# Performance work log

Measured on AMD Instinct MI355X. Metric: run time of the kernel, lower is better.

## Reference

```python
import jax, jax.numpy as jnp
import numpy as np

N_NODES = 50000
N_EDGES = 800000
D_IN = 128
D_HID = 128
D_OUT = 1
N_LAYERS = 3


def _sage_conv(x, src, dst, Wl, bl, Wr):
    # PyG SAGEConv (mean aggr): out = lin_l(mean_{j in N(i)} x_j) + lin_r(x_i)
    n = x.shape[0]
    msg = x[src]                                              # [E, F] gather
    s = jax.ops.segment_sum(msg, dst, num_segments=n)         # [N, F]
    cnt = jax.ops.segment_sum(jnp.ones((src.shape[0],), x.dtype), dst, num_segments=n)
    mean = s / jnp.maximum(cnt, 1.0)[:, None]
    return mean @ Wl.T + bl + x @ Wr.T


def setup_inputs() -> dict:
    key = jax.random.key(0)
    ks = jax.random.split(key, 2 + 3 * N_LAYERS + 2)
    x = jax.random.normal(ks[0], (N_NODES, D_IN), dtype=jnp.float32)
    edge_index = jax.random.randint(ks[1], (2, N_EDGES), 0, N_NODES, dtype=jnp.int64)
    inp = {"x": x, "edge_index": edge_index}
    dims_in = [D_IN] + [D_HID] * (N_LAYERS - 1)
    for i in range(N_LAYERS):
        fi = dims_in[i]
        sc = 1.0 / np.sqrt(fi)
        inp[f"Wl{i}"] = jax.random.uniform(ks[2 + 3 * i], (D_HID, fi), jnp.float32, -sc, sc)
        inp[f"bl{i}"] = jax.random.uniform(ks[3 + 3 * i], (D_HID,), jnp.float32, -sc, sc)
        inp[f"Wr{i}"] = jax.random.uniform(ks[4 + 3 * i], (D_HID, fi), jnp.float32, -sc, sc)
    sc = 1.0 / np.sqrt(D_HID)
    inp["Wf"] = jax.random.uniform(ks[-2], (D_OUT, D_HID), jnp.float32, -sc, sc)
    inp["bf"] = jax.random.uniform(ks[-1], (D_OUT,), jnp.float32, -sc, sc)
    return inp


def reference(x, edge_index, Wl0, bl0, Wr0, Wl1, bl1, Wr1, Wl2, bl2, Wr2, Wf, bf):
    src, dst = edge_index[0], edge_index[1]
    h = x
    # dropout is identity in eval mode (F.dropout with training=False)
    for Wl, bl, Wr in ((Wl0, bl0, Wr0), (Wl1, bl1, Wr1), (Wl2, bl2, Wr2)):
        h = jax.nn.relu(_sage_conv(h, src, dst, Wl, bl, Wr))
    return h @ Wf.T + bf
```

## Files before the change

### kernel.cpp

```cpp
#include <hip/hip_runtime.h>
#include <hip/hip_bf16.h>


constexpr int NN = 50000;
constexpr int NE = 800000;
constexpr int NTILE = NN / 16;
constexpr int EPB = 4096;
constexpr int NBLK = (NE + EPB - 1) / EPB;
constexpr int NBUCK = 196;
constexpr int BCAP = 6144;

using bf16x8 = __attribute__((ext_vector_type(8))) short;
using f32x4  = __attribute__((ext_vector_type(4))) float;

__device__ __forceinline__ unsigned short bf16_rne(float f) {
    unsigned u = __float_as_uint(f);
    unsigned r = (u + 0x7FFFu + ((u >> 16) & 1u)) >> 16;
    return (unsigned short)r;
}
__device__ __forceinline__ float bf16_f(unsigned short h) {
    return __uint_as_float(((unsigned)h) << 16);
}
__device__ __forceinline__ unsigned pack_split(float v) {
    unsigned short hi = bf16_rne(v);
    float r = v - bf16_f(hi);
    unsigned short lo = bf16_rne(r);
    return (((unsigned)hi) << 16) | (unsigned)lo;
}


__global__ __launch_bounds__(256) void k_hist(const int* __restrict__ ei,
                                              int* __restrict__ hist) {
    __shared__ int h[256];
    h[threadIdx.x] = 0;
    __syncthreads();
    int e0 = blockIdx.x * EPB;
    int e1 = e0 + EPB; if (e1 > NE) e1 = NE;
    for (int e = e0 + threadIdx.x; e < e1; e += 256)
        atomicAdd(&h[ei[NE + e] >> 8], 1);
    __syncthreads();
    hist[blockIdx.x * 256 + threadIdx.x] = h[threadIdx.x];
}

__global__ __launch_bounds__(256) void k_colscan(int* __restrict__ hist,
                                                 int* __restrict__ tot) {
    __shared__ int ws[4];
    int b = blockIdx.x;
    int t = threadIdx.x;
    int orig = (t < NBLK) ? hist[t * 256 + b] : 0;
    int v = orig;
    int lane = t & 63, wave = t >> 6;
    for (int o = 1; o < 64; o <<= 1) { int u = __shfl_up(v, o); if (lane >= o) v += u; }
    if (lane == 63) ws[wave] = v;
    __syncthreads();
    int off = 0;
    for (int w = 0; w < wave; ++w) off += ws[w];
    int st = v + off - orig;
    if (t < NBLK) hist[t * 256 + b] = st;
    if (t == 255) tot[b] = st + orig;
}

__global__ __launch_bounds__(256) void k_total(const int* __restrict__ tot,
                                               int* __restrict__ dbase) {
    __shared__ int ws[4];
    int t = threadIdx.x;
    int orig = tot[t];
    int v = orig;
    int lane = t & 63, wave = t >> 6;
    for (int o = 1; o < 64; o <<= 1) { int u = __shfl_up(v, o); if (lane >= o) v += u; }
    if (lane == 63) ws[wave] = v;
    __syncthreads();
    int off = 0;
    for (int w = 0; w < wave; ++w) off += ws[w];
    dbase[t] = v + off - orig;
    if (t == 255) dbase[256] = v + off;
}

__global__ __launch_bounds__(256) void k_addbase(int* __restrict__ hist,
                                                 const int* __restrict__ dbase) {
    hist[blockIdx.x * 256 + threadIdx.x] += dbase[threadIdx.x];
}

__global__ __launch_bounds__(256) void k_scatter1(const int* __restrict__ ei,
                                                  const int* __restrict__ hist,
                                                  unsigned* __restrict__ packed) {
    __shared__ int cur[256];
    cur[threadIdx.x] = hist[blockIdx.x * 256 + threadIdx.x];
    __syncthreads();
    int e0 = blockIdx.x * EPB;
    int e1 = e0 + EPB; if (e1 > NE) e1 = NE;
    for (int e = e0 + threadIdx.x; e < e1; e += 256) {
        int s = ei[e];
        int d = ei[NE + e];
        int pos = atomicAdd(&cur[d >> 8], 1);
        packed[pos] = ((unsigned)d << 16) | (unsigned)s;
    }
}

__global__ __launch_bounds__(256) void k_bucket_csr(const unsigned* __restrict__ packed,
        const int* __restrict__ dbase, unsigned short* __restrict__ perm,
        int* __restrict__ cnt, int* __restrict__ row_start) {
    __shared__ unsigned recs[BCAP];
    __shared__ unsigned short outs[BCAP];
    __shared__ int cntL[256];
    __shared__ int ws[4];
    int b = blockIdx.x;
    int lo = dbase[b];
    int m = dbase[b + 1] - lo;
    if (m > BCAP) m = BCAP;
    int t = threadIdx.x;
    cntL[t] = 0;
    __syncthreads();
    for (int i = t; i < m; i += 256) {
        unsigned r = packed[lo + i];
        recs[i] = r;
        atomicAdd(&cntL[(r >> 16) & 255], 1);
    }
    __syncthreads();
    int lane = t & 63, wave = t >> 6;
    int orig = cntL[t], v = orig;
    for (int o = 1; o < 64; o <<= 1) { int u = __shfl_up(v, o); if (lane >= o) v += u; }
    if (lane == 63) ws[wave] = v;
    __syncthreads();
    int off = 0;
    for (int w = 0; w < wave; ++w) off += ws[w];
    int st = v + off - orig;
    int node = b * 256 + t;
    if (node < NN) { cnt[node] = orig; row_start[node] = lo + st; }
    __syncthreads();
    cntL[t] = st;
    __syncthreads();
    for (int i = t; i < m; i += 256) {
        unsigned r = recs[i];
        int pos = atomicAdd(&cntL[(r >> 16) & 255], 1);
        outs[pos] = (unsigned short)(r & 0xFFFFu);
    }
    __syncthreads();
    for (int i = t; i < m; i += 256)
        perm[lo + i] = outs[i];
}


__global__ void k_pack_x(const float* __restrict__ x,
                         unsigned short* __restrict__ hhi,
                         unsigned short* __restrict__ hlo) {
    int i = blockIdx.x * blockDim.x + threadIdx.x;
    constexpr int TOT = NN * 128 / 4;
    if (i < TOT) {
        float4 v = ((const float4*)x)[i];
        unsigned p0 = pack_split(v.x), p1 = pack_split(v.y);
        unsigned p2 = pack_split(v.z), p3 = pack_split(v.w);
        uint2 hi, lo;
        hi.x = (p0 >> 16) | (p1 & 0xFFFF0000u);
        hi.y = (p2 >> 16) | (p3 & 0xFFFF0000u);
        lo.x = (p0 & 0xFFFFu) | (p1 << 16);
        lo.y = (p2 & 0xFFFFu) | (p3 << 16);
        ((uint2*)hhi)[i] = hi;
        ((uint2*)hlo)[i] = lo;
    }
}

__global__ void k_pack_w(const float* __restrict__ Wl, const float* __restrict__ Wr,
                         unsigned short* __restrict__ whi, unsigned short* __restrict__ wlo) {
    int i = blockIdx.x * blockDim.x + threadIdx.x;
    if (i < 128 * 256) {
        int c = i >> 8;
        int k = i & 255;
        float v = (k < 128) ? Wl[c * 128 + k] : Wr[c * 128 + (k - 128)];
        unsigned short hi = bf16_rne(v);
        whi[i] = hi;
        wlo[i] = bf16_rne(v - bf16_f(hi));
    }
}

__global__ void k_init_out(float* __restrict__ out, const float* __restrict__ bf) {
    int i = blockIdx.x * blockDim.x + threadIdx.x;
    if (i < NN) out[i] = bf[0];
}

__global__ __launch_bounds__(256) void k_aggregate(const unsigned short* __restrict__ hhi,
        const int* __restrict__ row_start, const int* __restrict__ cnt,
        const unsigned short* __restrict__ perm,
        unsigned short* __restrict__ shi, unsigned short* __restrict__ slo) {
    int wave = __builtin_amdgcn_readfirstlane(threadIdx.x >> 6);
    int lane = threadIdx.x & 63;
    int node = blockIdx.x * 4 + wave;
    if (node >= NN) return;
    int deg = cnt[node];
    int start = row_start[node];
    const unsigned* base = (const unsigned*)hhi;
    float ax = 0.f, ay = 0.f;
    int j = 0;
    for (; j + 16 <= deg; j += 16) {
        int s[16];
#pragma unroll
        for (int u = 0; u < 16; ++u) s[u] = perm[start + j + u];
        unsigned q[16];
#pragma unroll
        for (int u = 0; u < 16; ++u) q[u] = base[(size_t)s[u] * 64 + lane];
#pragma unroll
        for (int u = 0; u < 16; ++u) {
            ax += __uint_as_float(q[u] << 16);
            ay += __uint_as_float(q[u] & 0xFFFF0000u);
        }
    }
    for (; j + 4 <= deg; j += 4) {
        int s[4];
#pragma unroll
        for (int u = 0; u < 4; ++u) s[u] = perm[start + j + u];
        unsigned q[4];
#pragma unroll
        for (int u = 0; u < 4; ++u) q[u] = base[(size_t)s[u] * 64 + lane];
#pragma unroll
        for (int u = 0; u < 4; ++u) {
            ax += __uint_as_float(q[u] << 16);
            ay += __uint_as_float(q[u] & 0xFFFF0000u);
        }
    }
    for (; j < deg; ++j) {
        int s = perm[start + j];
        unsigned q = base[(size_t)s * 64 + lane];
        ax += __uint_as_float(q << 16);
        ay += __uint_as_float(q & 0xFFFF0000u);
    }
    float inv = 1.0f / (float)(deg > 1 ? deg : 1);
    unsigned p0 = pack_split(ax * inv);
    unsigned p1 = pack_split(ay * inv);
    ((unsigned*)shi)[(size_t)node * 64 + lane] = (p0 >> 16) | (p1 & 0xFFFF0000u);
    ((unsigned*)slo)[(size_t)node * 64 + lane] = (p0 & 0xFFFFu) | (p1 << 16);
}

__global__ __launch_bounds__(256, 2) void k_gemm_ws(
        const unsigned short* __restrict__ Ahi0, const unsigned short* __restrict__ Alo0,
        const unsigned short* __restrict__ Ahi1, const unsigned short* __restrict__ Alo1,
        const unsigned short* __restrict__ Whi, const unsigned short* __restrict__ Wlo,
        const float* __restrict__ bias,
        unsigned short* __restrict__ Ohi, unsigned short* __restrict__ Olo) {
    int wave = __builtin_amdgcn_readfirstlane(threadIdx.x >> 6);
    int lane = threadIdx.x & 63;
    int row = lane & 15;
    int kb = lane >> 4;
    int ct0 = wave * 2;

    bf16x8 bh[2][8], bl[2][8];
#pragma unroll
    for (int c = 0; c < 2; ++c)
#pragma unroll
        for (int kc = 0; kc < 8; ++kc) {
            size_t widx = (size_t)((ct0 + c) * 16 + row) * 256 + kc * 32 + kb * 8;
            bh[c][kc] = *(const bf16x8*)(Whi + widx);
            bl[c][kc] = *(const bf16x8*)(Wlo + widx);
        }
    float b0 = bias[ct0 * 16 + row];
    float b1 = bias[ct0 * 16 + 16 + row];

    for (int t = blockIdx.x; t < NTILE; t += gridDim.x) {
        int n0 = t * 16;
        size_t rb = (size_t)(n0 + row) * 128 + kb * 8;
        bf16x8 ah[8], al[8];
#pragma unroll
        for (int kc = 0; kc < 4; ++kc) {
            ah[kc] = *(const bf16x8*)(Ahi0 + rb + kc * 32);
            al[kc] = *(const bf16x8*)(Alo0 + rb + kc * 32);
        }
#pragma unroll
        for (int kc = 0; kc < 4; ++kc) {
            ah[4 + kc] = *(const bf16x8*)(Ahi1 + rb + kc * 32);
            al[4 + kc] = *(const bf16x8*)(Alo1 + rb + kc * 32);
        }
        f32x4 acc0 = {0.f, 0.f, 0.f, 0.f};
        f32x4 acc1 = {0.f, 0.f, 0.f, 0.f};
#pragma unroll
        for (int kc = 0; kc < 8; ++kc) {
            acc0 = __builtin_amdgcn_mfma_f32_16x16x32_bf16(ah[kc], bh[0][kc], acc0, 0, 0, 0);
            acc0 = __builtin_amdgcn_mfma_f32_16x16x32_bf16(al[kc], bh[0][kc], acc0, 0, 0, 0);
            acc0 = __builtin_amdgcn_mfma_f32_16x16x32_bf16(ah[kc], bl[0][kc], acc0, 0, 0, 0);
            acc1 = __builtin_amdgcn_mfma_f32_16x16x32_bf16(ah[kc], bh[1][kc], acc1, 0, 0, 0);
            acc1 = __builtin_amdgcn_mfma_f32_16x16x32_bf16(al[kc], bh[1][kc], acc1, 0, 0, 0);
            acc1 = __builtin_amdgcn_mfma_f32_16x16x32_bf16(ah[kc], bl[1][kc], acc1, 0, 0, 0);
        }
        __syncthreads();
        int cb0 = ct0 * 16 + row;
#pragma unroll
        for (int r = 0; r < 4; ++r) {
            int n = n0 + kb * 4 + r;
            size_t ro = (size_t)n * 128;
            unsigned p0 = pack_split(fmaxf(acc0[r] + b0, 0.f));
            unsigned p1 = pack_split(fmaxf(acc1[r] + b1, 0.f));
            Ohi[ro + cb0]      = (unsigned short)(p0 >> 16);
            Olo[ro + cb0]      = (unsigned short)(p0 & 0xFFFFu);
            Ohi[ro + cb0 + 16] = (unsigned short)(p1 >> 16);
            Olo[ro + cb0 + 16] = (unsigned short)(p1 & 0xFFFFu);
        }
    }
}

__global__ __launch_bounds__(256, 2) void k_gemm_head(
        const unsigned short* __restrict__ Ahi0, const unsigned short* __restrict__ Alo0,
        const unsigned short* __restrict__ Ahi1, const unsigned short* __restrict__ Alo1,
        const unsigned short* __restrict__ Whi, const unsigned short* __restrict__ Wlo,
        const float* __restrict__ bias, const float* __restrict__ Wf,
        float* __restrict__ out) {
    int wave = __builtin_amdgcn_readfirstlane(threadIdx.x >> 6);
    int lane = threadIdx.x & 63;
    int row = lane & 15;
    int kb = lane >> 4;
    int ct0 = wave * 2;

    bf16x8 bh[2][8], bl[2][8];
#pragma unroll
    for (int c = 0; c < 2; ++c)
#pragma unroll
        for (int kc = 0; kc < 8; ++kc) {
            size_t widx = (size_t)((ct0 + c) * 16 + row) * 256 + kc * 32 + kb * 8;
            bh[c][kc] = *(const bf16x8*)(Whi + widx);
            bl[c][kc] = *(const bf16x8*)(Wlo + widx);
        }
    float b0 = bias[ct0 * 16 + row];
    float b1 = bias[ct0 * 16 + 16 + row];
    float w0 = Wf[ct0 * 16 + row];
    float w1 = Wf[ct0 * 16 + 16 + row];

    for (int t = blockIdx.x; t < NTILE; t += gridDim.x) {
        int n0 = t * 16;
        size_t rb = (size_t)(n0 + row) * 128 + kb * 8;
        bf16x8 ah[8], al[8];
#pragma unroll
        for (int kc = 0; kc < 4; ++kc) {
            ah[kc] = *(const bf16x8*)(Ahi0 + rb + kc * 32);
            al[kc] = *(const bf16x8*)(Alo0 + rb + kc * 32);
        }
#pragma unroll
        for (int kc = 0; kc < 4; ++kc) {
            ah[4 + kc] = *(const bf16x8*)(Ahi1 + rb + kc * 32);
            al[4 + kc] = *(const bf16x8*)(Alo1 + rb + kc * 32);
        }
        f32x4 acc0 = {0.f, 0.f, 0.f, 0.f};
        f32x4 acc1 = {0.f, 0.f, 0.f, 0.f};
#pragma unroll
        for (int kc = 0; kc < 8; ++kc) {
            acc0 = __builtin_amdgcn_mfma_f32_16x16x32_bf16(ah[kc], bh[0][kc], acc0, 0, 0, 0);
            acc0 = __builtin_amdgcn_mfma_f32_16x16x32_bf16(al[kc], bh[0][kc], acc0, 0, 0, 0);
            acc0 = __builtin_amdgcn_mfma_f32_16x16x32_bf16(ah[kc], bl[0][kc], acc0, 0, 0, 0);
            acc1 = __builtin_amdgcn_mfma_f32_16x16x32_bf16(ah[kc], bh[1][kc], acc1, 0, 0, 0);
            acc1 = __builtin_amdgcn_mfma_f32_16x16x32_bf16(al[kc], bh[1][kc], acc1, 0, 0, 0);
            acc1 = __builtin_amdgcn_mfma_f32_16x16x32_bf16(ah[kc], bl[1][kc], acc1, 0, 0, 0);
        }
        float part[4];
#pragma unroll
        for (int r = 0; r < 4; ++r)
            part[r] = fmaxf(acc0[r] + b0, 0.f) * w0 + fmaxf(acc1[r] + b1, 0.f) * w1;
#pragma unroll
        for (int o = 1; o < 16; o <<= 1) {
#pragma unroll
            for (int r = 0; r < 4; ++r) part[r] += __shfl_xor(part[r], o);
        }
        if (row == 0) {
#pragma unroll
            for (int r = 0; r < 4; ++r) atomicAdd(&out[n0 + kb * 4 + r], part[r]);
        }
    }
}

extern "C" void kernel_launch(void* const* d_in, const int* in_sizes, int n_in,
                              void* d_out, int out_size, void* d_ws, size_t ws_size,
                              hipStream_t stream) {
    const float* x   = (const float*)d_in[0];
    const int*   ei  = (const int*)d_in[1];
    const float* Wl0 = (const float*)d_in[2];
    const float* bl0 = (const float*)d_in[3];
    const float* Wr0 = (const float*)d_in[4];
    const float* Wl1 = (const float*)d_in[5];
    const float* bl1 = (const float*)d_in[6];
    const float* Wr1 = (const float*)d_in[7];
    const float* Wl2 = (const float*)d_in[8];
    const float* bl2 = (const float*)d_in[9];
    const float* Wr2 = (const float*)d_in[10];
    const float* Wf  = (const float*)d_in[11];
    const float* bf  = (const float*)d_in[12];
    float* out = (float*)d_out;

    char* p = (char*)d_ws;
    auto alloc = [&](size_t n) { void* r = (void*)p; p += (n + 255) & ~(size_t)255; return r; };
    int*            hist      = (int*)alloc((size_t)NBLK * 256 * 4);
    int*            tot       = (int*)alloc(256 * 4);
    int*            dbase     = (int*)alloc(257 * 4);
    int*            cnt       = (int*)alloc((size_t)NN * 4);
    int*            row_start = (int*)alloc((size_t)NN * 4);
    unsigned short* perm      = (unsigned short*)alloc((size_t)NE * 2);
    unsigned short* s_hi      = (unsigned short*)alloc((size_t)NN * 128 * 2);
    unsigned short* s_lo      = (unsigned short*)alloc((size_t)NN * 128 * 2);
    unsigned short* h_hi      = (unsigned short*)alloc((size_t)NN * 128 * 2);
    unsigned short* h_lo      = (unsigned short*)alloc((size_t)NN * 128 * 2);
    unsigned short* whi       = (unsigned short*)alloc((size_t)3 * 128 * 256 * 2);
    unsigned short* wlo       = (unsigned short*)alloc((size_t)3 * 128 * 256 * 2);
    unsigned*       packed    = (unsigned*)s_hi;

    dim3 b256(256);
    k_hist<<<dim3(NBLK), b256, 0, stream>>>(ei, hist);
    k_colscan<<<dim3(256), b256, 0, stream>>>(hist, tot);
    k_total<<<dim3(1), b256, 0, stream>>>(tot, dbase);
    k_addbase<<<dim3(NBLK), b256, 0, stream>>>(hist, dbase);
    k_scatter1<<<dim3(NBLK), b256, 0, stream>>>(ei, hist, packed);
    k_bucket_csr<<<dim3(NBUCK), b256, 0, stream>>>(packed, dbase, perm, cnt, row_start);

    k_pack_x<<<dim3((NN * 128 / 4 + 255) / 256), b256, 0, stream>>>(x, h_hi, h_lo);
    k_pack_w<<<dim3(128), b256, 0, stream>>>(Wl0, Wr0, whi + 0 * 32768, wlo + 0 * 32768);
    k_pack_w<<<dim3(128), b256, 0, stream>>>(Wl1, Wr1, whi + 1 * 32768, wlo + 1 * 32768);
    k_pack_w<<<dim3(128), b256, 0, stream>>>(Wl2, Wr2, whi + 2 * 32768, wlo + 2 * 32768);
    k_init_out<<<dim3((NN + 255) / 256), b256, 0, stream>>>(out, bf);

    dim3 gAgg((NN + 3) / 4);
    dim3 gGemm(512);

    k_aggregate<<<gAgg, b256, 0, stream>>>(h_hi, row_start, cnt, perm, s_hi, s_lo);
    k_gemm_ws<<<gGemm, b256, 0, stream>>>(s_hi, s_lo, h_hi, h_lo,
                                          whi + 0 * 32768, wlo + 0 * 32768, bl0, h_hi, h_lo);
    k_aggregate<<<gAgg, b256, 0, stream>>>(h_hi, row_start, cnt, perm, s_hi, s_lo);
    k_gemm_ws<<<gGemm, b256, 0, stream>>>(s_hi, s_lo, h_hi, h_lo,
                                          whi + 1 * 32768, wlo + 1 * 32768, bl1, h_hi, h_lo);
    k_aggregate<<<gAgg, b256, 0, stream>>>(h_hi, row_start, cnt, perm, s_hi, s_lo);
    k_gemm_head<<<gGemm, b256, 0, stream>>>(s_hi, s_lo, h_hi, h_lo,
                                            whi + 2 * 32768, wlo + 2 * 32768, bl2, Wf, out);
}
```

Baseline: 334.5 us.

## Use fixed-capacity atomic buckets and padded vectorized neighbor gather in aggregation

The CSR build drops the histogram, column-scan, total and add-base kernels. Each edge block now reserves space in fixed-capacity per-bucket regions through global atomics, staging records in shared memory, and the output init is folded into a new init kernel. Neighbor lists are padded to multiples of eight using a zeroed sentinel row at index NN. This lets the aggregate kernel read neighbor indices as 16-byte vectors and have each half-wave gather a different neighbor with 8-byte loads, combining the halves with a cross-lane shuffle. The aim is fewer launches and fewer, wider memory instructions in the gather, at the cost of redundant gathers of the padding row and a reliance on bucket sizes staying under the fixed capacity.

```diff
diff --git a/kernel.cpp b/kernel.cpp
--- a/kernel.cpp
+++ b/kernel.cpp
@@ -9,6 +9,7 @@
 constexpr int NBLK = (NE + EPB - 1) / EPB;
 constexpr int NBUCK = 196;
 constexpr int BCAP = 6144;
+constexpr int PCAP = 6144;
 
 using bf16x8 = __attribute__((ext_vector_type(8))) short;
 using f32x4  = __attribute__((ext_vector_type(4))) float;
@@ -29,88 +30,57 @@
 }
 
 
-__global__ __launch_bounds__(256) void k_hist(const int* __restrict__ ei,
-                                              int* __restrict__ hist) {
+__global__ __launch_bounds__(256) void k_init(float* __restrict__ out,
+        const float* __restrict__ bf, int* __restrict__ bcnt,
+        unsigned short* __restrict__ hhi) {
+    int i = blockIdx.x * blockDim.x + threadIdx.x;
+    if (i < NN) out[i] = bf[0];
+    if (i < 256) bcnt[i] = 0;
+    if (i < 128) hhi[(size_t)NN * 128 + i] = 0;
+}
+
+
+__global__ __launch_bounds__(256) void k_build_buckets(const int* __restrict__ ei,
+        int* __restrict__ bcnt, unsigned* __restrict__ packed) {
+    __shared__ unsigned stage[EPB];
     __shared__ int h[256];
-    h[threadIdx.x] = 0;
+    __shared__ int cur[256];
+    int t = threadIdx.x;
+    h[t] = 0;
     __syncthreads();
     int e0 = blockIdx.x * EPB;
     int e1 = e0 + EPB; if (e1 > NE) e1 = NE;
-    for (int e = e0 + threadIdx.x; e < e1; e += 256)
-        atomicAdd(&h[ei[NE + e] >> 8], 1);
-    __syncthreads();
-    hist[blockIdx.x * 256 + threadIdx.x] = h[threadIdx.x];
-}
-
-__global__ __launch_bounds__(256) void k_colscan(int* __restrict__ hist,
-                                                 int* __restrict__ tot) {
-    __shared__ int ws[4];
-    int b = blockIdx.x;
-    int t = threadIdx.x;
-    int orig = (t < NBLK) ? hist[t * 256 + b] : 0;
-    int v = orig;
-    int lane = t & 63, wave = t >> 6;
-    for (int o = 1; o < 64; o <<= 1) { int u = __shfl_up(v, o); if (lane >= o) v += u; }
-    if (lane == 63) ws[wave] = v;
-    __syncthreads();
-    int off = 0;
-    for (int w = 0; w < wave; ++w) off += ws[w];
-    int st = v + off - orig;
-    if (t < NBLK) hist[t * 256 + b] = st;
-    if (t == 255) tot[b] = st + orig;
-}
-
-__global__ __launch_bounds__(256) void k_total(const int* __restrict__ tot,
-                                               int* __restrict__ dbase) {
-    __shared__ int ws[4];
-    int t = threadIdx.x;
-    int orig = tot[t];
-    int v = orig;
-    int lane = t & 63, wave = t >> 6;
-    for (int o = 1; o < 64; o <<= 1) { int u = __shfl_up(v, o); if (lane >= o) v += u; }
-    if (lane == 63) ws[wave] = v;
-    __syncthreads();
-    int off = 0;
-    for (int w = 0; w < wave; ++w) off += ws[w];
-    dbase[t] = v + off - orig;
-    if (t == 255) dbase[256] = v + off;
-}
-
-__global__ __launch_bounds__(256) void k_addbase(int* __restrict__ hist,
-                                                 const int* __restrict__ dbase) {
-    hist[blockIdx.x * 256 + threadIdx.x] += dbase[threadIdx.x];
-}
-
-__global__ __launch_bounds__(256) void k_scatter1(const int* __restrict__ ei,
-                                                  const int* __restrict__ hist,
-                                                  unsigned* __restrict__ packed) {
-    __shared__ int cur[256];
-    cur[threadIdx.x] = hist[blockIdx.x * 256 + threadIdx.x];
-    __syncthreads();
-    int e0 = blockIdx.x * EPB;
-    int e1 = e0 + EPB; if (e1 > NE) e1 = NE;
-    for (int e = e0 + threadIdx.x; e < e1; e += 256) {
+    for (int e = e0 + t; e < e1; e += 256) {
         int s = ei[e];
         int d = ei[NE + e];
-        int pos = atomicAdd(&cur[d >> 8], 1);
-        packed[pos] = ((unsigned)d << 16) | (unsigned)s;
+        stage[e - e0] = ((unsigned)d << 16) | (unsigned)s;
+        atomicAdd(&h[d >> 8], 1);
+    }
+    __syncthreads();
+    if (t < NBUCK) cur[t] = t * BCAP + atomicAdd(&bcnt[t], h[t]);
+    __syncthreads();
+    for (int e = e0 + t; e < e1; e += 256) {
+        unsigned r = stage[e - e0];
+        int pos = atomicAdd(&cur[r >> 24], 1);
+        packed[pos] = r;
     }
 }
 
 __global__ __launch_bounds__(256) void k_bucket_csr(const unsigned* __restrict__ packed,
-        const int* __restrict__ dbase, unsigned short* __restrict__ perm,
+        const int* __restrict__ bcnt, unsigned short* __restrict__ perm,
         int* __restrict__ cnt, int* __restrict__ row_start) {
     __shared__ unsigned recs[BCAP];
-    __shared__ unsigned short outs[BCAP];
+    __shared__ unsigned short outs[PCAP];
     __shared__ int cntL[256];
     __shared__ int ws[4];
+    __shared__ int totS;
     int b = blockIdx.x;
-    int lo = dbase[b];
-    int m = dbase[b + 1] - lo;
+    int m = bcnt[b];
     if (m > BCAP) m = BCAP;
     int t = threadIdx.x;
     cntL[t] = 0;
     __syncthreads();
+    int lo = b * BCAP;
     for (int i = t; i < m; i += 256) {
         unsigned r = packed[lo + i];
         recs[i] = r;
@@ -118,15 +88,18 @@
     }
     __syncthreads();
     int lane = t & 63, wave = t >> 6;
-    int orig = cntL[t], v = orig;
+    int orig = cntL[t];
+    int pc = (orig + 7) & ~7;
+    int v = pc;
     for (int o = 1; o < 64; o <<= 1) { int u = __shfl_up(v, o); if (lane >= o) v += u; }
     if (lane == 63) ws[wave] = v;
     __syncthreads();
     int off = 0;
     for (int w = 0; w < wave; ++w) off += ws[w];
-    int st = v + off - orig;
+    int st = v + off - pc;
     int node = b * 256 + t;
-    if (node < NN) { cnt[node] = orig; row_start[node] = lo + st; }
+    if (node < NN) { cnt[node] = orig; row_start[node] = b * PCAP + st; }
+    if (t == 255) totS = st + pc;
     __syncthreads();
     cntL[t] = st;
     __syncthreads();
@@ -135,9 +108,11 @@
         int pos = atomicAdd(&cntL[(r >> 16) & 255], 1);
         outs[pos] = (unsigned short)(r & 0xFFFFu);
     }
-    __syncthreads();
-    for (int i = t; i < m; i += 256)
-        perm[lo + i] = outs[i];
+    for (int i = st + orig; i < st + pc; ++i) outs[i] = (unsigned short)NN;
+    __syncthreads();
+    int totp = totS;
+    for (int i = t; i < totp; i += 256)
+        perm[b * PCAP + i] = outs[i];
 }
 
 
@@ -173,11 +148,6 @@
     }
 }
 
-__global__ void k_init_out(float* __restrict__ out, const float* __restrict__ bf) {
-    int i = blockIdx.x * blockDim.x + threadIdx.x;
-    if (i < NN) out[i] = bf[0];
-}
-
 __global__ __launch_bounds__(256) void k_aggregate(const unsigned short* __restrict__ hhi,
         const int* __restrict__ row_start, const int* __restrict__ cnt,
         const unsigned short* __restrict__ perm,
@@ -188,46 +158,65 @@
     if (node >= NN) return;
     int deg = cnt[node];
     int start = row_start[node];
-    const unsigned* base = (const unsigned*)hhi;
-    float ax = 0.f, ay = 0.f;
+    int h16 = (lane >> 5) << 4;
+    int c8  = (lane & 31) << 3;
+    const char* base = (const char*)hhi;
+    float a0 = 0.f, a1 = 0.f, a2 = 0.f, a3 = 0.f;
+    int pdeg = (deg + 7) & ~7;
+    const uint4* pp = (const uint4*)(perm + start);
     int j = 0;
-    for (; j + 16 <= deg; j += 16) {
-        int s[16];
-#pragma unroll
-        for (int u = 0; u < 16; ++u) s[u] = perm[start + j + u];
-        unsigned q[16];
-#pragma unroll
-        for (int u = 0; u < 16; ++u) q[u] = base[(size_t)s[u] * 64 + lane];
-#pragma unroll
-        for (int u = 0; u < 16; ++u) {
-            ax += __uint_as_float(q[u] << 16);
-            ay += __uint_as_float(q[u] & 0xFFFF0000u);
-        }
-    }
-    for (; j + 4 <= deg; j += 4) {
-        int s[4];
-#pragma unroll
-        for (int u = 0; u < 4; ++u) s[u] = perm[start + j + u];
-        unsigned q[4];
-#pragma unroll
-        for (int u = 0; u < 4; ++u) q[u] = base[(size_t)s[u] * 64 + lane];
+    for (; j + 16 <= pdeg; j += 16) {
+        uint4 w0 = pp[0], w1 = pp[1]; pp += 2;
+        unsigned pw[8] = {w0.x, w0.y, w0.z, w0.w, w1.x, w1.y, w1.z, w1.w};
+        uint2 q[8];
+#pragma unroll
+        for (int u = 0; u < 8; ++u) {
+            unsigned src = (pw[u] >> h16) & 0xFFFFu;
+            q[u] = *(const uint2*)(base + ((size_t)src << 8) + c8);
+        }
+#pragma unroll
+        for (int u = 0; u < 8; ++u) {
+            a0 += __uint_as_float(q[u].x << 16);
+            a1 += __uint_as_float(q[u].x & 0xFFFF0000u);
+            a2 += __uint_as_float(q[u].y << 16);
+            a3 += __uint_as_float(q[u].y & 0xFFFF0000u);
+        }
+    }
+    if (j < pdeg) {
+        uint4 w0 = *pp;
+        unsigned pw[4] = {w0.x, w0.y, w0.z, w0.w};
+        uint2 q[4];
 #pragma unroll
         for (int u = 0; u < 4; ++u) {
-            ax += __uint_as_float(q[u] << 16);
-            ay += __uint_as_float(q[u] & 0xFFFF0000u);
-        }
-    }
-    for (; j < deg; ++j) {
-        int s = perm[start + j];
-        unsigned q = base[(size_t)s * 64 + lane];
-        ax += __uint_as_float(q << 16);
-        ay += __uint_as_float(q & 0xFFFF0000u);
-    }
+            unsigned src = (pw[u] >> h16) & 0xFFFFu;
+            q[u] = *(const uint2*)(base + ((size_t)src << 8) + c8);
+        }
+#pragma unroll
+        for (int u = 0; u < 4; ++u) {
+            a0 += __uint_as_float(q[u].x << 16);
+            a1 += __uint_as_float(q[u].x & 0xFFFF0000u);
+            a2 += __uint_as_float(q[u].y << 16);
+            a3 += __uint_as_float(q[u].y & 0xFFFF0000u);
+        }
+    }
+    a0 += __shfl_xor(a0, 32);
+    a1 += __shfl_xor(a1, 32);
+    a2 += __shfl_xor(a2, 32);
+    a3 += __shfl_xor(a3, 32);
     float inv = 1.0f / (float)(deg > 1 ? deg : 1);
-    unsigned p0 = pack_split(ax * inv);
-    unsigned p1 = pack_split(ay * inv);
-    ((unsigned*)shi)[(size_t)node * 64 + lane] = (p0 >> 16) | (p1 & 0xFFFF0000u);
-    ((unsigned*)slo)[(size_t)node * 64 + lane] = (p0 & 0xFFFFu) | (p1 << 16);
+    unsigned p0 = pack_split(a0 * inv);
+    unsigned p1 = pack_split(a1 * inv);
+    unsigned p2 = pack_split(a2 * inv);
+    unsigned p3 = pack_split(a3 * inv);
+    if (lane < 32) {
+        uint2 hi, lo;
+        hi.x = (p0 >> 16) | (p1 & 0xFFFF0000u);
+        hi.y = (p2 >> 16) | (p3 & 0xFFFF0000u);
+        lo.x = (p0 & 0xFFFFu) | (p1 << 16);
+        lo.y = (p2 & 0xFFFFu) | (p3 << 16);
+        ((uint2*)shi)[(size_t)node * 32 + lane] = hi;
+        ((uint2*)slo)[(size_t)node * 32 + lane] = lo;
+    }
 }
 
 __global__ __launch_bounds__(256, 2) void k_gemm_ws(
@@ -382,33 +371,27 @@
 
     char* p = (char*)d_ws;
     auto alloc = [&](size_t n) { void* r = (void*)p; p += (n + 255) & ~(size_t)255; return r; };
-    int*            hist      = (int*)alloc((size_t)NBLK * 256 * 4);
-    int*            tot       = (int*)alloc(256 * 4);
-    int*            dbase     = (int*)alloc(257 * 4);
+    int*            bcnt      = (int*)alloc(256 * 4);
     int*            cnt       = (int*)alloc((size_t)NN * 4);
     int*            row_start = (int*)alloc((size_t)NN * 4);
-    unsigned short* perm      = (unsigned short*)alloc((size_t)NE * 2);
-    unsigned short* s_hi      = (unsigned short*)alloc((size_t)NN * 128 * 2);
-    unsigned short* s_lo      = (unsigned short*)alloc((size_t)NN * 128 * 2);
-    unsigned short* h_hi      = (unsigned short*)alloc((size_t)NN * 128 * 2);
-    unsigned short* h_lo      = (unsigned short*)alloc((size_t)NN * 128 * 2);
+    unsigned short* perm      = (unsigned short*)alloc((size_t)NBUCK * PCAP * 2);
+    unsigned short* s_hi      = (unsigned short*)alloc((size_t)(NN + 1) * 128 * 2);
+    unsigned short* s_lo      = (unsigned short*)alloc((size_t)(NN + 1) * 128 * 2);
+    unsigned short* h_hi      = (unsigned short*)alloc((size_t)(NN + 1) * 128 * 2);
+    unsigned short* h_lo      = (unsigned short*)alloc((size_t)(NN + 1) * 128 * 2);
     unsigned short* whi       = (unsigned short*)alloc((size_t)3 * 128 * 256 * 2);
     unsigned short* wlo       = (unsigned short*)alloc((size_t)3 * 128 * 256 * 2);
     unsigned*       packed    = (unsigned*)s_hi;
 
     dim3 b256(256);
-    k_hist<<<dim3(NBLK), b256, 0, stream>>>(ei, hist);
-    k_colscan<<<dim3(256), b256, 0, stream>>>(hist, tot);
-    k_total<<<dim3(1), b256, 0, stream>>>(tot, dbase);
-    k_addbase<<<dim3(NBLK), b256, 0, stream>>>(hist, dbase);
-    k_scatter1<<<dim3(NBLK), b256, 0, stream>>>(ei, hist, packed);
-    k_bucket_csr<<<dim3(NBUCK), b256, 0, stream>>>(packed, dbase, perm, cnt, row_start);
+    k_init<<<dim3((NN + 255) / 256), b256, 0, stream>>>(out, bf, bcnt, h_hi);
+    k_build_buckets<<<dim3(NBLK), b256, 0, stream>>>(ei, bcnt, packed);
+    k_bucket_csr<<<dim3(NBUCK), b256, 0, stream>>>(packed, bcnt, perm, cnt, row_start);
 
     k_pack_x<<<dim3((NN * 128 / 4 + 255) / 256), b256, 0, stream>>>(x, h_hi, h_lo);
     k_pack_w<<<dim3(128), b256, 0, stream>>>(Wl0, Wr0, whi + 0 * 32768, wlo + 0 * 32768);
     k_pack_w<<<dim3(128), b256, 0, stream>>>(Wl1, Wr1, whi + 1 * 32768, wlo + 1 * 32768);
     k_pack_w<<<dim3(128), b256, 0, stream>>>(Wl2, Wr2, whi + 2 * 32768, wlo + 2 * 32768);
-    k_init_out<<<dim3((NN + 255) / 256), b256, 0, stream>>>(out, bf);
 
     dim3 gAgg((NN + 3) / 4);
     dim3 gGemm(512);
```

Result: faster. 312.9 us (-6.5%).
